# Kernel optimization log

Hardware: AMD Instinct MI355X
Metric: run time of the kernel (lower is better)

The kernel has to match this reference:

```python
import jax, jax.numpy as jnp
import numpy as np

B, N, D, HID, OUT = 4, 6144, 64, 512, 64
FINE_CONF = 0.25


def setup_inputs() -> dict:
    key = jax.random.key(0)
    ks = jax.random.split(key, 16)

    def unit(k, shape):
        v = jax.random.normal(k, shape, dtype=jnp.float32)
        return v / jnp.linalg.norm(v, axis=-1, keepdims=True)

    def lin(k, fan_in, shape):
        return jax.random.normal(k, shape, dtype=jnp.float32) * (1.0 / np.sqrt(fan_in))

    return {
        'feats1': unit(ks[0], (B, N, D)),
        'feats2': unit(ks[1], (B, N, D)),
        'kps1': jax.random.uniform(ks[2], (B, N, 2), dtype=jnp.float32) * 512.0,
        'kps2': jax.random.uniform(ks[3], (B, N, 2), dtype=jnp.float32) * 512.0,
        'scales1': jnp.ones((B, N), dtype=jnp.float32),
        'w1': lin(ks[4], 2 * D, (2 * D, HID)), 'b1': jnp.zeros((HID,), jnp.float32),
        'w2': lin(ks[5], HID, (HID, HID)),   'b2': jnp.zeros((HID,), jnp.float32),
        'w3': lin(ks[6], HID, (HID, HID)),   'b3': jnp.zeros((HID,), jnp.float32),
        'w4': lin(ks[7], HID, (HID, HID)),   'b4': jnp.zeros((HID,), jnp.float32),
        'w5': lin(ks[8], HID, (HID, OUT)),   'b5': jnp.zeros((OUT,), jnp.float32),
    }


def _fine_matcher(x, w1, b1, w2, b2, w3, b3, w4, b4, w5, b5):
    # eval-mode BN folded into the Linears -> plain MLP
    h = jax.nn.relu(x @ w1 + b1)
    h = jax.nn.relu(h @ w2 + b2)
    h = jax.nn.relu(h @ w3 + b3)
    h = jax.nn.relu(h @ w4 + b4)
    return h @ w5 + b5  # [B, N, 64]


def reference(feats1, feats2, kps1, kps2, scales1,
              w1, b1, w2, b2, w3, b3, w4, b4, w5, b5):
    # ---- batch_match: dense cosine sim + bidirectional argmax + mutual check ----
    cossim = jnp.einsum('bnd,bmd->bnm', feats1, feats2)       # [B, N, N]
    match12 = jnp.argmax(cossim, axis=-1)                      # [B, N]
    match21 = jnp.argmax(cossim, axis=1)                       # [B, N] (argmax over rows)
    idx0 = jnp.arange(match12.shape[1])
    back = jnp.take_along_axis(match21, match12, axis=1)       # match21[match12]
    mutual = back == idx0[None, :]                             # [B, N] bool

    # ---- refine_matches (masked instead of boolean compaction, jit-friendly) ----
    f2 = jnp.take_along_axis(feats2, match12[..., None], axis=1)   # [B, N, D]
    mkpts1 = jnp.take_along_axis(kps2, match12[..., None], axis=1) # [B, N, 2]
    offsets_raw = _fine_matcher(jnp.concatenate([feats1, f2], axis=-1),
                                w1, b1, w2, b2, w3, b3, w4, b4, w5, b5)  # [B, N, 64]

    # conf = softmax(3*offsets).max ; subpix uses softmax(3*offsets) too (temp=3)
    heat = jax.nn.softmax(3.0 * offsets_raw, axis=-1)          # [B, N, 64]
    conf = jnp.max(heat, axis=-1)                              # [B, N]

    hm = heat.reshape(heat.shape[0], heat.shape[1], 8, 8)      # [B, N, Hh, Wh]
    g = jnp.arange(8, dtype=heat.dtype) - 4.0                  # x - W//2 / y - H//2
    coords_x = jnp.sum(hm * g[None, None, None, :], axis=(-1, -2))
    coords_y = jnp.sum(hm * g[None, None, :, None], axis=(-1, -2))
    offsets = jnp.stack([coords_x, coords_y], axis=-1)         # [B, N, 2]

    mkpts0 = kps1 + offsets * scales1[..., None]
    matches = jnp.concatenate([mkpts0, mkpts1], axis=-1)       # [B, N, 4]
    mask_good = mutual & (conf > FINE_CONF)                    # valid-match mask
    return matches, mask_good
```

## Files before the change

### kernel.cpp

```cpp
#include <hip/hip_runtime.h>
#include <cstddef>
#include <cstdint>

#define BB 4
#define NN 6144
#define DD 64
#define HID 512
#define OUTD 64
#define CAP 512
#define RSPLIT 2

typedef unsigned long long ull;
typedef unsigned int u32;
typedef unsigned short u16;
typedef unsigned char u8;
typedef __attribute__((ext_vector_type(8))) short short8_t;
typedef __attribute__((ext_vector_type(4))) float floatx4;

#define OFF_ROWFIN 0
#define OFF_COLFIN 196608
#define OFF_WT     393216
#define OFF_F1T    2162688
#define OFF_F2T    5308416
#define OFF_RBM    8454144
#define OFF_CBM    10813440
#define OFF_CNTR   13172736
#define OFF_CNTC   13173504
#define OFF_LISTR  13174272
#define OFF_LISTC  13567488

#define WT1_OFF 0
#define WT2_OFF 65536
#define WT3_OFF 327680
#define WT4_OFF 589824
#define WT5_OFF 851968
#define WT_TOTAL 884736

__device__ __forceinline__ unsigned int fkey(float v) {
    unsigned int u = __float_as_uint(v);
    return (u & 0x80000000u) ? ~u : (u | 0x80000000u);
}

__device__ __forceinline__ float inv16(u32 k16) {
    u32 u = k16 << 16;
    return (u & 0x80000000u) ? __uint_as_float(u & 0x7fffffffu)
                             : __uint_as_float(~u);
}

__device__ __forceinline__ u16 f2bf(float f) {
    unsigned int u = __float_as_uint(f);
    u += 0x7FFFu + ((u >> 16) & 1u);
    return (u16)(u >> 16);
}

__device__ __forceinline__ u32 f2fp8x2(float a, float b) {
    return (u32)__builtin_amdgcn_cvt_pk_fp8_f32(a, b, 0, false) & 0xffffu;
}

__global__ __launch_bounds__(256) void prep_kernel(
    const float* __restrict__ w1, const float* __restrict__ w2,
    const float* __restrict__ w3, const float* __restrict__ w4,
    const float* __restrict__ w5,
    const float* __restrict__ f1, const float* __restrict__ f2,
    u8* __restrict__ wt8, u16* __restrict__ f1t, u16* __restrict__ f2t,
    ull* __restrict__ finals, int* __restrict__ cnts)
{
    int idx = blockIdx.x * 256 + threadIdx.x;

    if (idx < 2 * BB * NN) finals[idx] = 0ULL;
    if (idx < 384) cnts[idx] = 0;

    if (idx < WT_TOTAL) {
        const float* w; u8* o; int K, nsh, li;
        if (idx < 65536)        { w = w1; o = wt8 + WT1_OFF; K = 128; nsh = 9; li = idx; }
        else if (idx < 327680)  { w = w2; o = wt8 + WT2_OFF; K = 512; nsh = 9; li = idx - 65536; }
        else if (idx < 589824)  { w = w3; o = wt8 + WT3_OFF; K = 512; nsh = 9; li = idx - 327680; }
        else if (idx < 851968)  { w = w4; o = wt8 + WT4_OFF; K = 512; nsh = 9; li = idx - 589824; }
        else                    { w = w5; o = wt8 + WT5_OFF; K = 512; nsh = 6; li = idx - 851968; }
        int k = li >> nsh;
        int n = li & ((1 << nsh) - 1);
        u8 v = (u8)(f2fp8x2(w[li], 0.0f) & 0xff);
        int lane = (n & 15) | (((k >> 3) & 3) << 4);
        o[(((size_t)(n >> 4) * (K >> 5) + (k >> 5)) * 64 + lane) * 8 + (k & 7)] = v;
    }

    {
        const int TE = BB * NN * DD;
        const float* src; u16* dst; int e;
        if (idx < TE) { src = f1; dst = f1t; e = idx; }
        else          { src = f2; dst = f2t; e = idx - TE; }
        int k  = e & 63;
        int rn = e >> 6;
        int b  = rn / NN;
        int r  = rn - b * NN;
        int R  = r >> 7, rb = (r >> 4) & 7;
        int kb = k >> 5, lane = (r & 15) | (((k >> 3) & 3) << 4), j = k & 7;
        dst[(size_t)(b * 48 + R) * 8192 + ((rb * 2 + kb) * 64 + lane) * 8 + j] = f2bf(src[e]);
    }
}

__global__ __launch_bounds__(256, 4) void simb_kernel(
    const u16* __restrict__ f1t, const u16* __restrict__ f2t,
    u16* __restrict__ rbm, u16* __restrict__ cbm)
{
    __shared__ float cv[4][128];
    const int R = blockIdx.x, C = blockIdx.y, b = blockIdx.z;
    const int t = threadIdx.x, lane = t & 63, w = t >> 6;
    const int l15 = lane & 15, l4 = lane >> 4;

    const u16* At = f1t + (size_t)(b * 48 + R) * 8192;
    const u16* Bt = f2t + (size_t)(b * 48 + C) * 8192;

    short8_t afr[2][2];
    #pragma unroll
    for (int i = 0; i < 2; ++i)
        #pragma unroll
        for (int kb = 0; kb < 2; ++kb)
            afr[i][kb] = *reinterpret_cast<const short8_t*>(
                At + ((2 * w + i) * 2 + kb) * 512 + lane * 8);

    floatx4 acc[2][8];
    #pragma unroll
    for (int i = 0; i < 2; ++i)
        #pragma unroll
        for (int j = 0; j < 8; ++j) acc[i][j] = (floatx4)(0.0f);

    short8_t bc0 = *reinterpret_cast<const short8_t*>(Bt + lane * 8);
    short8_t bc1 = *reinterpret_cast<const short8_t*>(Bt + 512 + lane * 8);
    short8_t bn0, bn1;
    #pragma unroll
    for (int j = 0; j < 8; ++j) {
        if (j < 7) {
            bn0 = *reinterpret_cast<const short8_t*>(
                Bt + ((j + 1) * 2 + 0) * 512 + lane * 8);
            bn1 = *reinterpret_cast<const short8_t*>(
                Bt + ((j + 1) * 2 + 1) * 512 + lane * 8);
        }
        #pragma unroll
        for (int i = 0; i < 2; ++i)
            acc[i][j] = __builtin_amdgcn_mfma_f32_16x16x32_bf16(
                afr[i][0], bc0, acc[i][j], 0, 0, 0);
        #pragma unroll
        for (int i = 0; i < 2; ++i)
            acc[i][j] = __builtin_amdgcn_mfma_f32_16x16x32_bf16(
                afr[i][1], bc1, acc[i][j], 0, 0, 0);
        if (j < 7) { bc0 = bn0; bc1 = bn1; }
    }

    #pragma unroll
    for (int i = 0; i < 2; ++i) {
        #pragma unroll
        for (int reg = 0; reg < 4; ++reg) {
            float v = acc[i][0][reg];
            #pragma unroll
            for (int j = 1; j < 8; ++j) v = fmaxf(v, acc[i][j][reg]);
            v = fmaxf(v, __shfl_xor(v, 1));
            v = fmaxf(v, __shfl_xor(v, 2));
            v = fmaxf(v, __shfl_xor(v, 4));
            v = fmaxf(v, __shfl_xor(v, 8));
            if (l15 == 0) {
                int row = R * 128 + w * 32 + i * 16 + l4 * 4 + reg;
                rbm[((size_t)b * 48 + C) * NN + row] = (u16)(fkey(v) >> 16);
            }
        }
    }

    #pragma unroll
    for (int j = 0; j < 8; ++j) {
        float v = acc[0][j][0];
        #pragma unroll
        for (int i = 0; i < 2; ++i)
            #pragma unroll
            for (int reg = 0; reg < 4; ++reg) v = fmaxf(v, acc[i][j][reg]);
        v = fmaxf(v, __shfl_xor(v, 16));
        v = fmaxf(v, __shfl_xor(v, 32));
        if (l4 == 0) cv[w][j * 16 + l15] = v;
    }
    __syncthreads();
    if (t < 128) {
        float v = fmaxf(fmaxf(cv[0][t], cv[1][t]), fmaxf(cv[2][t], cv[3][t]));
        cbm[((size_t)b * 48 + R) * NN + C * 128 + t] = (u16)(fkey(v) >> 16);
    }
}

__global__ __launch_bounds__(256) void scan_kernel(
    const u16* __restrict__ rbm, const u16* __restrict__ cbm,
    int* __restrict__ cntR, int* __restrict__ cntC,
    int* __restrict__ listR, int* __restrict__ listC)
{
    const u16* bm = blockIdx.y ? cbm : rbm;
    int* cnt  = blockIdx.y ? cntC : cntR;
    int* list = blockIdx.y ? listC : listR;

    __shared__ int lcnt[48];
    __shared__ int lbase[48];
    const int t = threadIdx.x;
    if (t < 48) lcnt[t] = 0;
    const int idx = blockIdx.x * 256 + t;
    const int b = (blockIdx.x * 256) / NN;
    const int n = idx - b * NN;

    u16 ks[48];
    #pragma unroll
    for (int c = 0; c < 48; ++c)
        ks[c] = bm[((size_t)b * 48 + c) * NN + n];

    u16 mx = 0;
    #pragma unroll
    for (int c = 0; c < 48; ++c) mx = ks[c] > mx ? ks[c] : mx;
    float thr = inv16(mx) - 0.010f;
    u32 m0 = 0, m1 = 0;
    #pragma unroll
    for (int c = 0; c < 48; ++c) {
        if (inv16((u32)ks[c] + 1) >= thr) {
            if (c < 32) m0 |= 1u << c; else m1 |= 1u << (c - 32);
        }
    }
    __syncthreads();
    {
        u32 a = m0;
        while (a) { int c = __builtin_ctz(a); a &= a - 1; atomicAdd(&lcnt[c], 1); }
        a = m1;
        while (a) { int c = 32 + __builtin_ctz(a); a &= a - 1; atomicAdd(&lcnt[c], 1); }
    }
    __syncthreads();
    if (t < 48) { lbase[t] = atomicAdd(&cnt[b * 48 + t], lcnt[t]); lcnt[t] = 0; }
    __syncthreads();
    {
        u32 a = m0;
        while (a) {
            int c = __builtin_ctz(a); a &= a - 1;
            int pos = lbase[c] + atomicAdd(&lcnt[c], 1);
            if (pos < CAP) list[(b * 48 + c) * CAP + pos] = n;
        }
        a = m1;
        while (a) {
            int c = 32 + __builtin_ctz(a); a &= a - 1;
            int pos = lbase[c] + atomicAdd(&lcnt[c], 1);
            if (pos < CAP) list[(b * 48 + c) * CAP + pos] = n;
        }
    }
}

__global__ __launch_bounds__(256, 2) void refine_kernel(
    const float* __restrict__ f1, const float* __restrict__ f2,
    const int* __restrict__ cntR, const int* __restrict__ cntC,
    const int* __restrict__ listR, const int* __restrict__ listC,
    ull* __restrict__ rowfin, ull* __restrict__ colfin)
{
    const float* qfeat = blockIdx.z ? f2 : f1;
    const float* tfeat = blockIdx.z ? f1 : f2;
    const int* cnt  = blockIdx.z ? cntC : cntR;
    const int* list = blockIdx.z ? listC : listR;
    ull* fin = blockIdx.z ? colfin : rowfin;

    const int b = blockIdx.x / 48;
    const int C = blockIdx.x - b * 48;
    const int sub = blockIdx.y;
    int n_items = cnt[b * 48 + C];
    if (n_items > CAP) n_items = CAP;
    int chunk = (n_items + RSPLIT - 1) / RSPLIT;
    int lo = sub * chunk;
    int hi = lo + chunk; if (hi > n_items) hi = n_items;
    if (lo >= hi) return;

    __shared__ float s2f[128 * 68];
    __shared__ float sq[64 * 68];
    const int t = threadIdx.x;
    const int cg = t & 15;
    const int rs = t >> 4;
    const float* tb = tfeat + ((size_t)b * NN + C * 128) * 64;
    #pragma unroll
    for (int p = 0; p < 8; ++p) {
        int idx = p * 256 + t;
        int row = idx >> 4, c4 = idx & 15;
        *reinterpret_cast<float4*>(&s2f[row * 68 + c4 * 4]) =
            *reinterpret_cast<const float4*>(tb + row * 64 + c4 * 4);
    }
    __syncthreads();
    const int* mylist = list + (b * 48 + C) * CAP;

    for (int base = lo; base < hi; base += 64) {
        __syncthreads();
        #pragma unroll
        for (int s = 0; s < 4; ++s) {
            int fi = s * 256 + t;
            int q = fi >> 4, c4 = fi & 15;
            int lq = base + q;
            int nn = (lq < hi) ? mylist[lq] : mylist[lo];
            *reinterpret_cast<float4*>(&sq[q * 68 + c4 * 4]) =
                *reinterpret_cast<const float4*>(
                    qfeat + ((size_t)b * NN + nn) * 64 + c4 * 4);
        }
        __syncthreads();

        float acc[4][8];
        #pragma unroll
        for (int j = 0; j < 4; ++j)
            #pragma unroll
            for (int c8 = 0; c8 < 8; ++c8) acc[j][c8] = 0.0f;

        #pragma unroll 4
        for (int kq = 0; kq < 16; ++kq) {
            float4 qv[4];
            #pragma unroll
            for (int j = 0; j < 4; ++j)
                qv[j] = *reinterpret_cast<const float4*>(
                    &sq[(rs * 4 + j) * 68 + kq * 4]);
            #pragma unroll
            for (int c8 = 0; c8 < 8; ++c8) {
                float4 tv = *reinterpret_cast<const float4*>(
                    &s2f[(cg + 16 * c8) * 68 + kq * 4]);
                #pragma unroll
                for (int j = 0; j < 4; ++j) {
                    acc[j][c8] = fmaf(qv[j].x, tv.x, acc[j][c8]);
                    acc[j][c8] = fmaf(qv[j].y, tv.y, acc[j][c8]);
                    acc[j][c8] = fmaf(qv[j].z, tv.z, acc[j][c8]);
                    acc[j][c8] = fmaf(qv[j].w, tv.w, acc[j][c8]);
                }
            }
        }

        #pragma unroll
        for (int j = 0; j < 4; ++j) {
            int lq = base + rs * 4 + j;
            bool valid = lq < hi;
            float bv = acc[j][0]; int bt = cg;
            #pragma unroll
            for (int c8 = 1; c8 < 8; ++c8)
                if (acc[j][c8] > bv) { bv = acc[j][c8]; bt = cg + 16 * c8; }
            ull pk = ((ull)fkey(bv) << 32) | (u32)(~(u32)(C * 128 + bt));
            ull qq;
            qq = __shfl_xor(pk, 1); pk = pk > qq ? pk : qq;
            qq = __shfl_xor(pk, 2); pk = pk > qq ? pk : qq;
            qq = __shfl_xor(pk, 4); pk = pk > qq ? pk : qq;
            qq = __shfl_xor(pk, 8); pk = pk > qq ? pk : qq;
            if (cg == 0 && valid) {
                int n = mylist[lq];
                atomicMax(&fin[(size_t)b * NN + n], pk);
            }
        }
    }
}


#define MLP_STEP(BUF, KB)                                                        \
    {                                                                            \
        const int kb2 = ((KB) + woff) & (NKB - 1);                               \
        __builtin_amdgcn_s_setprio(1);                                           \
        _Pragma("unroll")                                                        \
        for (int jb = 0; jb < 6; ++jb) {                                         \
            const int pt = jb * 16 + l15;                                        \
            const int sp = (kb2 * 4 + l4) ^ (pt & 7);                            \
            long bfr = *reinterpret_cast<const long*>(act + pt * 512 + sp * 8);  \
            _Pragma("unroll")                                                    \
            for (int ia = 0; ia < 4; ++ia)                                       \
                acc[ia][jb] = __builtin_amdgcn_mfma_f32_16x16x32_fp8_fp8(        \
                    BUF[ia], bfr, acc[ia][jb], 0, 0, 0);                         \
        }                                                                        \
        __builtin_amdgcn_s_setprio(0);                                           \
        if ((KB) + 3 < NKB) {                                                    \
            const int kbp = ((KB) + 3 + woff) & (NKB - 1);                       \
            _Pragma("unroll")                                                    \
            for (int ia = 0; ia < 4; ++ia)                                       \
                BUF[ia] = *reinterpret_cast<const long*>(                        \
                    wt8 + (((size_t)(chBlk0 + ia) * NKB + kbp) * 64 + lane) * 8);\
        }                                                                        \
    }

template<int K>
__device__ __forceinline__ void mlp_layer8(
    u8* act, const u8* __restrict__ wt8,
    const float* __restrict__ bias, int lane, int wid)
{
    constexpr int NKB = K / 32;
    floatx4 acc[4][6];
    #pragma unroll
    for (int ia = 0; ia < 4; ++ia)
        #pragma unroll
        for (int jb = 0; jb < 6; ++jb)
            acc[ia][jb] = (floatx4)(0.0f);

    const int l15 = lane & 15, l4 = lane >> 4;
    const int chBlk0 = wid * 4;
    const int woff = (wid * 2) & (NKB - 1);

    long a0[4], a1[4], a2[4];
    #pragma unroll
    for (int ia = 0; ia < 4; ++ia)
        a0[ia] = *reinterpret_cast<const long*>(
            wt8 + (((size_t)(chBlk0 + ia) * NKB + ((0 + woff) & (NKB - 1))) * 64 + lane) * 8);
    #pragma unroll
    for (int ia = 0; ia < 4; ++ia)
        a1[ia] = *reinterpret_cast<const long*>(
            wt8 + (((size_t)(chBlk0 + ia) * NKB + ((1 + woff) & (NKB - 1))) * 64 + lane) * 8);
    #pragma unroll
    for (int ia = 0; ia < 4; ++ia)
        a2[ia] = *reinterpret_cast<const long*>(
            wt8 + (((size_t)(chBlk0 + ia) * NKB + ((2 + woff) & (NKB - 1))) * 64 + lane) * 8);

    #pragma unroll
    for (int kb = 0; kb < NKB; ++kb) {
        if ((kb % 3) == 0)      MLP_STEP(a0, kb)
        else if ((kb % 3) == 1) MLP_STEP(a1, kb)
        else                    MLP_STEP(a2, kb)
    }
    __syncthreads();

    const int ch0 = wid * 64;
    #pragma unroll
    for (int ia = 0; ia < 4; ++ia) {
        int cb = ia * 16 + l4 * 4;
        float4 bv = *reinterpret_cast<const float4*>(bias + ch0 + cb);
        #pragma unroll
        for (int jb = 0; jb < 6; ++jb) {
            int pt = jb * 16 + l15;
            u32 pk0 = f2fp8x2(fmaxf(acc[ia][jb][0] + bv.x, 0.0f),
                              fmaxf(acc[ia][jb][1] + bv.y, 0.0f));
            u32 pk1 = f2fp8x2(fmaxf(acc[ia][jb][2] + bv.z, 0.0f),
                              fmaxf(acc[ia][jb][3] + bv.w, 0.0f));
            u32 word = pk0 | (pk1 << 16);
            int s = (ch0 + cb) >> 3;
            int sp = s ^ (pt & 7);
            *reinterpret_cast<u32*>(act + pt * 512 + sp * 8 + (cb & 4)) = word;
        }
    }
    __syncthreads();
}

__global__ __launch_bounds__(512, 2) void mlp_mfma_kernel(
    const float* __restrict__ f1, const float* __restrict__ f2,
    const float* __restrict__ kps1, const float* __restrict__ kps2,
    const float* __restrict__ scales1,
    const float* __restrict__ b1, const float* __restrict__ b2,
    const float* __restrict__ b3, const float* __restrict__ b4,
    const float* __restrict__ b5,
    const u8* __restrict__ wt8,
    const ull* __restrict__ rowfin, const ull* __restrict__ colfin,
    float* __restrict__ out)
{
    __shared__ __align__(16) unsigned char lds_raw[49152];
    u8* act = lds_raw;
    float* logf = reinterpret_cast<float*>(lds_raw);

    const int t = threadIdx.x;
    const int lane = t & 63, wid = t >> 6;
    const int base = blockIdx.x * 96;
    const int b = base / NN;
    const int n0 = base % NN;

    if (t < 384) {
        const int pt = t >> 2, seg = t & 3;
        const int n = n0 + pt;
        ull rm = rowfin[(size_t)b * NN + n];
        const int m = (int)(~(u32)(rm & 0xffffffffULL));
        const float* src = (seg < 2)
            ? (f1 + ((size_t)b * NN + n) * DD + seg * 32)
            : (f2 + ((size_t)b * NN + m) * DD + (seg - 2) * 32);
        #pragma unroll
        for (int q8 = 0; q8 < 4; ++q8) {
            float4 v0 = *reinterpret_cast<const float4*>(src + q8 * 8);
            float4 v1 = *reinterpret_cast<const float4*>(src + q8 * 8 + 4);
            ull w64 = (ull)f2fp8x2(v0.x, v0.y)
                    | ((ull)f2fp8x2(v0.z, v0.w) << 16)
                    | ((ull)f2fp8x2(v1.x, v1.y) << 32)
                    | ((ull)f2fp8x2(v1.z, v1.w) << 48);
            int s = seg * 4 + q8;
            int sp = s ^ (pt & 7);
            *reinterpret_cast<ull*>(act + pt * 512 + sp * 8) = w64;
        }
    }
    __syncthreads();

    mlp_layer8<128>(act, wt8 + WT1_OFF, b1, lane, wid);
    mlp_layer8<512>(act, wt8 + WT2_OFF, b2, lane, wid);
    mlp_layer8<512>(act, wt8 + WT3_OFF, b3, lane, wid);
    mlp_layer8<512>(act, wt8 + WT4_OFF, b4, lane, wid);

    {
        const int l15 = lane & 15, l4 = lane >> 4;
        floatx4 acc5[6];
        #pragma unroll
        for (int jb = 0; jb < 6; ++jb) acc5[jb] = (floatx4)(0.0f);
        if (wid < 4) {
            const int woff5 = (wid * 4) & 15;
            long a_cur = *reinterpret_cast<const long*>(
                wt8 + WT5_OFF + (((size_t)wid * 16 + woff5) * 64 + lane) * 8);
            long a_nxt;
            #pragma unroll
            for (int kb = 0; kb < 16; ++kb) {
                const int kb2 = (kb + woff5) & 15;
                if (kb + 1 < 16) {
                    const int kbn = (kb + 1 + woff5) & 15;
                    a_nxt = *reinterpret_cast<const long*>(
                        wt8 + WT5_OFF + (((size_t)wid * 16 + kbn) * 64 + lane) * 8);
                }
                __builtin_amdgcn_s_setprio(1);
                #pragma unroll
                for (int jb = 0; jb < 6; ++jb) {
                    const int pt = jb * 16 + l15;
                    const int sp = (kb2 * 4 + l4) ^ (pt & 7);
                    long bfr = *reinterpret_cast<const long*>(act + pt * 512 + sp * 8);
                    acc5[jb] = __builtin_amdgcn_mfma_f32_16x16x32_fp8_fp8(
                        a_cur, bfr, acc5[jb], 0, 0, 0);
                }
                __builtin_amdgcn_s_setprio(0);
                if (kb + 1 < 16) a_cur = a_nxt;
            }
        }
        __syncthreads();
        if (wid < 4) {
            int cb = wid * 16 + l4 * 4;
            float4 bv = *reinterpret_cast<const float4*>(b5 + cb);
            #pragma unroll
            for (int jb = 0; jb < 6; ++jb) {
                int pt = jb * 16 + l15;
                float4 o;
                o.x = acc5[jb][0] + bv.x;
                o.y = acc5[jb][1] + bv.y;
                o.z = acc5[jb][2] + bv.z;
                o.w = acc5[jb][3] + bv.w;
                *reinterpret_cast<float4*>(&logf[pt * 68 + cb]) = o;
            }
        }
        __syncthreads();
    }

    if (t < 96) {
        const int pt = t;
        const int n = n0 + pt;
        const float* lrow = &logf[pt * 68];
        float mx = -1e30f;
        #pragma unroll 8
        for (int j = 0; j < OUTD; ++j) mx = fmaxf(mx, 3.0f * lrow[j]);
        float s = 0.0f, cx = 0.0f, cy = 0.0f;
        #pragma unroll 8
        for (int j = 0; j < OUTD; ++j) {
            float e = __expf(3.0f * lrow[j] - mx);
            s  += e;
            cx += e * (float)((j & 7) - 4);
            cy += e * (float)((j >> 3) - 4);
        }
        float conf = 1.0f / s;
        cx /= s; cy /= s;
        ull rm = rowfin[(size_t)b * NN + n];
        int m = (int)(~(u32)(rm & 0xffffffffULL));
        ull cm = colfin[(size_t)b * NN + m];
        int back = (int)(~(u32)(cm & 0xffffffffULL));
        bool mutual = (back == n);
        float sc = scales1[(size_t)b * NN + n];
        float x0 = kps1[((size_t)b * NN + n) * 2 + 0] + cx * sc;
        float y0 = kps1[((size_t)b * NN + n) * 2 + 1] + cy * sc;
        float x1 = kps2[((size_t)b * NN + m) * 2 + 0];
        float y1 = kps2[((size_t)b * NN + m) * 2 + 1];
        float* mt = out + ((size_t)b * NN + n) * 4;
        mt[0] = x0; mt[1] = y0; mt[2] = x1; mt[3] = y1;
        out[(size_t)BB * NN * 4 + (size_t)b * NN + n] =
            (mutual && conf > 0.25f) ? 1.0f : 0.0f;
    }
}

extern "C" void kernel_launch(void* const* d_in, const int* in_sizes, int n_in,
                              void* d_out, int out_size, void* d_ws, size_t ws_size,
                              hipStream_t stream)
{
    const float* f1  = (const float*)d_in[0];
    const float* f2  = (const float*)d_in[1];
    const float* kp1 = (const float*)d_in[2];
    const float* kp2 = (const float*)d_in[3];
    const float* sc1 = (const float*)d_in[4];
    const float* w1  = (const float*)d_in[5];
    const float* b1  = (const float*)d_in[6];
    const float* w2  = (const float*)d_in[7];
    const float* b2  = (const float*)d_in[8];
    const float* w3  = (const float*)d_in[9];
    const float* b3  = (const float*)d_in[10];
    const float* w4  = (const float*)d_in[11];
    const float* b4  = (const float*)d_in[12];
    const float* w5  = (const float*)d_in[13];
    const float* b5  = (const float*)d_in[14];

    char* ws = (char*)d_ws;
    ull* rowfin = (ull*)(ws + OFF_ROWFIN);
    ull* colfin = (ull*)(ws + OFF_COLFIN);
    u8*  wt8    = (u8*)(ws + OFF_WT);
    u16* f1t    = (u16*)(ws + OFF_F1T);
    u16* f2t    = (u16*)(ws + OFF_F2T);
    u16* rbm    = (u16*)(ws + OFF_RBM);
    u16* cbm    = (u16*)(ws + OFF_CBM);
    int* cntR   = (int*)(ws + OFF_CNTR);
    int* cntC   = (int*)(ws + OFF_CNTC);
    int* listR  = (int*)(ws + OFF_LISTR);
    int* listC  = (int*)(ws + OFF_LISTC);
    float* out  = (float*)d_out;

    prep_kernel<<<(2 * BB * NN * DD) / 256, 256, 0, stream>>>(
        w1, w2, w3, w4, w5, f1, f2, wt8, f1t, f2t, rowfin, cntR);

    dim3 gS(48, 48, BB);
    simb_kernel<<<gS, 256, 0, stream>>>(f1t, f2t, rbm, cbm);

    dim3 gScan((BB * NN) / 256, 2);
    scan_kernel<<<gScan, 256, 0, stream>>>(rbm, cbm, cntR, cntC, listR, listC);

    dim3 gR(BB * 48, RSPLIT, 2);
    refine_kernel<<<gR, 256, 0, stream>>>(f1, f2, cntR, cntC, listR, listC,
                                          rowfin, colfin);

    mlp_mfma_kernel<<<(BB * NN) / 96, 512, 0, stream>>>(
        f1, f2, kp1, kp2, sc1, b1, b2, b3, b4, b5, wt8, rowfin, colfin, out);
}
```

Before: 131.5 us.

## Double MLP block to 16 waves splitting points between wave pairs

The fused MLP kernel now launches 1024 threads per block instead of 512. Each pair of waves shares a 64-channel group, and each wave handles 48 of the 96 points, so per-wave accumulators shrink from 24 to 12 tiles. The aim is more waves per CU to hide LDS and weight-load latency, since the grid has only 256 blocks. The cost is that each weight fragment is loaded twice from global/L2, and launch bounds of 4 may cap registers and cause spills. The refine kernel's launch bounds minimum-blocks hint also goes from 2 to 4.

```diff
diff --git a/kernel.cpp b/kernel.cpp
--- a/kernel.cpp
+++ b/kernel.cpp
@@ -242,7 +242,7 @@
     }
 }
 
-__global__ __launch_bounds__(256, 2) void refine_kernel(
+__global__ __launch_bounds__(256, 4) void refine_kernel(
     const float* __restrict__ f1, const float* __restrict__ f2,
     const int* __restrict__ cntR, const int* __restrict__ cntC,
     const int* __restrict__ listR, const int* __restrict__ listC,
@@ -349,8 +349,8 @@
         const int kb2 = ((KB) + woff) & (NKB - 1);                               \
         __builtin_amdgcn_s_setprio(1);                                           \
         _Pragma("unroll")                                                        \
-        for (int jb = 0; jb < 6; ++jb) {                                         \
-            const int pt = jb * 16 + l15;                                        \
+        for (int jb = 0; jb < 3; ++jb) {                                         \
+            const int pt = p0 + jb * 16 + l15;                                   \
             const int sp = (kb2 * 4 + l4) ^ (pt & 7);                            \
             long bfr = *reinterpret_cast<const long*>(act + pt * 512 + sp * 8);  \
             _Pragma("unroll")                                                    \
@@ -369,20 +369,22 @@
     }
 
 template<int K>
-__device__ __forceinline__ void mlp_layer8(
+__device__ __forceinline__ void mlp_layer16(
     u8* act, const u8* __restrict__ wt8,
     const float* __restrict__ bias, int lane, int wid)
 {
     constexpr int NKB = K / 32;
-    floatx4 acc[4][6];
+    floatx4 acc[4][3];
     #pragma unroll
     for (int ia = 0; ia < 4; ++ia)
         #pragma unroll
-        for (int jb = 0; jb < 6; ++jb)
+        for (int jb = 0; jb < 3; ++jb)
             acc[ia][jb] = (floatx4)(0.0f);
 
     const int l15 = lane & 15, l4 = lane >> 4;
-    const int chBlk0 = wid * 4;
+    const int chg = wid >> 1;
+    const int p0  = (wid & 1) * 48;
+    const int chBlk0 = chg * 4;
     const int woff = (wid * 2) & (NKB - 1);
 
     long a0[4], a1[4], a2[4];
@@ -407,14 +409,14 @@
     }
     __syncthreads();
 
-    const int ch0 = wid * 64;
+    const int ch0 = chg * 64;
     #pragma unroll
     for (int ia = 0; ia < 4; ++ia) {
         int cb = ia * 16 + l4 * 4;
         float4 bv = *reinterpret_cast<const float4*>(bias + ch0 + cb);
         #pragma unroll
-        for (int jb = 0; jb < 6; ++jb) {
-            int pt = jb * 16 + l15;
+        for (int jb = 0; jb < 3; ++jb) {
+            int pt = p0 + jb * 16 + l15;
             u32 pk0 = f2fp8x2(fmaxf(acc[ia][jb][0] + bv.x, 0.0f),
                               fmaxf(acc[ia][jb][1] + bv.y, 0.0f));
             u32 pk1 = f2fp8x2(fmaxf(acc[ia][jb][2] + bv.z, 0.0f),
@@ -428,7 +430,7 @@
     __syncthreads();
 }
 
-__global__ __launch_bounds__(512, 2) void mlp_mfma_kernel(
+__global__ __launch_bounds__(1024, 4) void mlp_mfma_kernel(
     const float* __restrict__ f1, const float* __restrict__ f2,
     const float* __restrict__ kps1, const float* __restrict__ kps2,
     const float* __restrict__ scales1,
@@ -472,20 +474,22 @@
     }
     __syncthreads();
 
-    mlp_layer8<128>(act, wt8 + WT1_OFF, b1, lane, wid);
-    mlp_layer8<512>(act, wt8 + WT2_OFF, b2, lane, wid);
-    mlp_layer8<512>(act, wt8 + WT3_OFF, b3, lane, wid);
-    mlp_layer8<512>(act, wt8 + WT4_OFF, b4, lane, wid);
+    mlp_layer16<128>(act, wt8 + WT1_OFF, b1, lane, wid);
+    mlp_layer16<512>(act, wt8 + WT2_OFF, b2, lane, wid);
+    mlp_layer16<512>(act, wt8 + WT3_OFF, b3, lane, wid);
+    mlp_layer16<512>(act, wt8 + WT4_OFF, b4, lane, wid);
 
     {
         const int l15 = lane & 15, l4 = lane >> 4;
-        floatx4 acc5[6];
-        #pragma unroll
-        for (int jb = 0; jb < 6; ++jb) acc5[jb] = (floatx4)(0.0f);
-        if (wid < 4) {
+        floatx4 acc5[3];
+        #pragma unroll
+        for (int jb = 0; jb < 3; ++jb) acc5[jb] = (floatx4)(0.0f);
+        if (wid < 8) {
+            const int chg5 = wid >> 1;
+            const int p0 = (wid & 1) * 48;
             const int woff5 = (wid * 4) & 15;
             long a_cur = *reinterpret_cast<const long*>(
-                wt8 + WT5_OFF + (((size_t)wid * 16 + woff5) * 64 + lane) * 8);
+                wt8 + WT5_OFF + (((size_t)chg5 * 16 + woff5) * 64 + lane) * 8);
             long a_nxt;
             #pragma unroll
             for (int kb = 0; kb < 16; ++kb) {
@@ -493,12 +497,12 @@
                 if (kb + 1 < 16) {
                     const int kbn = (kb + 1 + woff5) & 15;
                     a_nxt = *reinterpret_cast<const long*>(
-                        wt8 + WT5_OFF + (((size_t)wid * 16 + kbn) * 64 + lane) * 8);
+                        wt8 + WT5_OFF + (((size_t)chg5 * 16 + kbn) * 64 + lane) * 8);
                 }
                 __builtin_amdgcn_s_setprio(1);
                 #pragma unroll
-                for (int jb = 0; jb < 6; ++jb) {
-                    const int pt = jb * 16 + l15;
+                for (int jb = 0; jb < 3; ++jb) {
+                    const int pt = p0 + jb * 16 + l15;
                     const int sp = (kb2 * 4 + l4) ^ (pt & 7);
                     long bfr = *reinterpret_cast<const long*>(act + pt * 512 + sp * 8);
                     acc5[jb] = __builtin_amdgcn_mfma_f32_16x16x32_fp8_fp8(
@@ -509,12 +513,14 @@
             }
         }
         __syncthreads();
-        if (wid < 4) {
-            int cb = wid * 16 + l4 * 4;
+        if (wid < 8) {
+            const int chg5 = wid >> 1;
+            const int p0 = (wid & 1) * 48;
+            int cb = chg5 * 16 + l4 * 4;
             float4 bv = *reinterpret_cast<const float4*>(b5 + cb);
             #pragma unroll
-            for (int jb = 0; jb < 6; ++jb) {
-                int pt = jb * 16 + l15;
+            for (int jb = 0; jb < 3; ++jb) {
+                int pt = p0 + jb * 16 + l15;
                 float4 o;
                 o.x = acc5[jb][0] + bv.x;
                 o.y = acc5[jb][1] + bv.y;
@@ -607,6 +613,6 @@
     refine_kernel<<<gR, 256, 0, stream>>>(f1, f2, cntR, cntC, listR, listC,
                                           rowfin, colfin);
 
-    mlp_mfma_kernel<<<(BB * NN) / 96, 512, 0, stream>>>(
+    mlp_mfma_kernel<<<(BB * NN) / 96, 1024, 0, stream>>>(
         f1, f2, kp1, kp2, sc1, b1, b2, b3, b4, b5, wt8, rowfin, colfin, out);
 }
```

New measurement: 165.0 us. +25.5%, slower.
